# Performance work log

Measured on AMD Instinct MI355X. Metric: run time of the kernel, lower is better.

Reference implementation:

```python
import jax, jax.numpy as jnp
import numpy as np

IN_FEATURES = 4096
OUT_FEATURES = 4096
BATCH = 16384


def setup_inputs() -> dict:
    key = jax.random.key(0)
    k_x, k_w, k_b = jax.random.split(key, 3)
    x = jax.random.normal(k_x, (BATCH, IN_FEATURES), dtype=jnp.float32)
    # nn.Linear default init: U(-1/sqrt(in), 1/sqrt(in))
    bound = 1.0 / np.sqrt(IN_FEATURES)
    W = jax.random.uniform(k_w, (OUT_FEATURES, IN_FEATURES), dtype=jnp.float32,
                           minval=-bound, maxval=bound)
    bias = jax.random.uniform(k_b, (OUT_FEATURES,), dtype=jnp.float32,
                              minval=-bound, maxval=bound)
    return {"x": x, "W": W, "bias": bias}


def reference(x, W, bias):
    # Algebraic reduction: sum_j (x @ W.T + b)[i, j]
    #   = x @ sum_j W[j, :] + sum_j b[j]
    weight_sums = jnp.sum(W, axis=0)          # [in_features]
    bias_sum = jnp.sum(bias)                  # scalar
    out = x @ weight_sums + bias_sum          # [batch]
    return out[:, None]                       # [batch, 1]
```

## Files before the change

kernel.cpp:

```cpp
#include <hip/hip_runtime.h>

#define IN_F 4096
#define OUT_F 4096
#define BATCH 16384


__global__ __launch_bounds__(256) void colsum_kernel(
    const float* __restrict__ W, const float* __restrict__ bias,
    float* __restrict__ ws) {
  const int ROWS_PER_CHUNK = OUT_F / 64;
  int col4 = blockIdx.x * 256 + threadIdx.x;
  int row0 = blockIdx.y * ROWS_PER_CHUNK;
  const float4* W4 = (const float4*)W;

  float4 acc = make_float4(0.f, 0.f, 0.f, 0.f);
  #pragma unroll 8
  for (int r = 0; r < ROWS_PER_CHUNK; ++r) {
    float4 v = W4[(size_t)(row0 + r) * (IN_F / 4) + col4];
    acc.x += v.x; acc.y += v.y; acc.z += v.z; acc.w += v.w;
  }
  atomicAdd(&ws[col4 * 4 + 0], acc.x);
  atomicAdd(&ws[col4 * 4 + 1], acc.y);
  atomicAdd(&ws[col4 * 4 + 2], acc.z);
  atomicAdd(&ws[col4 * 4 + 3], acc.w);

  if (blockIdx.x == 0 && blockIdx.y == 0) {
    float b = 0.f;
    for (int i = threadIdx.x; i < OUT_F; i += 256) b += bias[i];
    #pragma unroll
    for (int off = 32; off > 0; off >>= 1) b += __shfl_down(b, off);
    if ((threadIdx.x & 63) == 0) atomicAdd(&ws[IN_F], b);
  }
}

__global__ __launch_bounds__(256) void rowdot_kernel(
    const float* __restrict__ x, const float* __restrict__ ws,
    float* __restrict__ out) {
  __shared__ float4 sw[IN_F / 4];
  __shared__ float sbias;

  const float4* ws4 = (const float4*)ws;
  for (int i = threadIdx.x; i < IN_F / 4; i += 256) sw[i] = ws4[i];
  if (threadIdx.x == 0) sbias = ws[IN_F];
  __syncthreads();

  int wave = threadIdx.x >> 6;
  int lane = threadIdx.x & 63;
  int row  = blockIdx.x * 4 + wave;

  const float4* xr = (const float4*)(x + (size_t)row * IN_F);
  float acc = 0.f;
  #pragma unroll
  for (int it = 0; it < IN_F / 4 / 64; ++it) {
    float4 xv = xr[it * 64 + lane];
    float4 wv = sw[it * 64 + lane];
    acc += xv.x * wv.x + xv.y * wv.y + xv.z * wv.z + xv.w * wv.w;
  }
  #pragma unroll
  for (int off = 32; off > 0; off >>= 1) acc += __shfl_down(acc, off);
  if (lane == 0) out[row] = acc + sbias;
}

extern "C" void kernel_launch(void* const* d_in, const int* in_sizes, int n_in,
                              void* d_out, int out_size, void* d_ws, size_t ws_size,
                              hipStream_t stream) {
  const float* x    = (const float*)d_in[0];
  const float* W    = (const float*)d_in[1];
  const float* bias = (const float*)d_in[2];
  float* out = (float*)d_out;
  float* ws  = (float*)d_ws;

  hipMemsetAsync(ws, 0, (IN_F + 1) * sizeof(float), stream);

  dim3 g1(4, 64);
  colsum_kernel<<<g1, 256, 0, stream>>>(W, bias, ws);

  rowdot_kernel<<<BATCH / 4, 256, 0, stream>>>(x, ws, out);
}
```

Before: 401.3 us.

## Process four rows per wave in rowdot and split colsum over more blocks

The row-dot kernel now has each wave compute four output rows at once. Each shared-memory weight load is reused across four x rows, and more independent global loads are in flight per thread. The colsum kernel uses 16-row chunks across 256 y-blocks instead of 64-row chunks, raising parallelism for the W reduction at the cost of four times as many atomics. The grid for rowdot shrinks to 1024 blocks, which lowers the number of blocks per CU on the memory-bound 256 MB read of x.

```diff
diff --git a/kernel.cpp b/kernel.cpp
--- a/kernel.cpp
+++ b/kernel.cpp
@@ -8,13 +8,13 @@
 __global__ __launch_bounds__(256) void colsum_kernel(
     const float* __restrict__ W, const float* __restrict__ bias,
     float* __restrict__ ws) {
-  const int ROWS_PER_CHUNK = OUT_F / 64;
+  const int ROWS_PER_CHUNK = 16;
   int col4 = blockIdx.x * 256 + threadIdx.x;
   int row0 = blockIdx.y * ROWS_PER_CHUNK;
   const float4* W4 = (const float4*)W;
 
   float4 acc = make_float4(0.f, 0.f, 0.f, 0.f);
-  #pragma unroll 8
+  #pragma unroll
   for (int r = 0; r < ROWS_PER_CHUNK; ++r) {
     float4 v = W4[(size_t)(row0 + r) * (IN_F / 4) + col4];
     acc.x += v.x; acc.y += v.y; acc.z += v.z; acc.w += v.w;
@@ -46,19 +46,39 @@
 
   int wave = threadIdx.x >> 6;
   int lane = threadIdx.x & 63;
-  int row  = blockIdx.x * 4 + wave;
+  int row0 = (blockIdx.x * 4 + wave) * 4;
 
-  const float4* xr = (const float4*)(x + (size_t)row * IN_F);
-  float acc = 0.f;
-  #pragma unroll
-  for (int it = 0; it < IN_F / 4 / 64; ++it) {
-    float4 xv = xr[it * 64 + lane];
-    float4 wv = sw[it * 64 + lane];
-    acc += xv.x * wv.x + xv.y * wv.y + xv.z * wv.z + xv.w * wv.w;
+  const int LD = IN_F / 4;
+  const float4* x0 = (const float4*)(x + (size_t)row0 * IN_F);
+
+  float a0 = 0.f, a1 = 0.f, a2 = 0.f, a3 = 0.f;
+  #pragma unroll 4
+  for (int it = 0; it < 16; ++it) {
+    int o = it * 64 + lane;
+    float4 wv = sw[o];
+    float4 v0 = x0[o];
+    float4 v1 = x0[o + LD];
+    float4 v2 = x0[o + 2 * LD];
+    float4 v3 = x0[o + 3 * LD];
+    a0 += v0.x * wv.x + v0.y * wv.y + v0.z * wv.z + v0.w * wv.w;
+    a1 += v1.x * wv.x + v1.y * wv.y + v1.z * wv.z + v1.w * wv.w;
+    a2 += v2.x * wv.x + v2.y * wv.y + v2.z * wv.z + v2.w * wv.w;
+    a3 += v3.x * wv.x + v3.y * wv.y + v3.z * wv.z + v3.w * wv.w;
   }
   #pragma unroll
-  for (int off = 32; off > 0; off >>= 1) acc += __shfl_down(acc, off);
-  if (lane == 0) out[row] = acc + sbias;
+  for (int off = 32; off > 0; off >>= 1) {
+    a0 += __shfl_down(a0, off);
+    a1 += __shfl_down(a1, off);
+    a2 += __shfl_down(a2, off);
+    a3 += __shfl_down(a3, off);
+  }
+  if (lane == 0) {
+    float b = sbias;
+    out[row0 + 0] = a0 + b;
+    out[row0 + 1] = a1 + b;
+    out[row0 + 2] = a2 + b;
+    out[row0 + 3] = a3 + b;
+  }
 }
 
 extern "C" void kernel_launch(void* const* d_in, const int* in_sizes, int n_in,
@@ -72,8 +92,8 @@
 
   hipMemsetAsync(ws, 0, (IN_F + 1) * sizeof(float), stream);
 
-  dim3 g1(4, 64);
+  dim3 g1(4, 256);
   colsum_kernel<<<g1, 256, 0, stream>>>(W, bias, ws);
 
-  rowdot_kernel<<<BATCH / 4, 256, 0, stream>>>(x, ws, out);
+  rowdot_kernel<<<BATCH / 16, 256, 0, stream>>>(x, ws, out);
 }
```

Measured after the change: 415.8 us. +3.6%, slower.
